# Kernel optimization log

Hardware: AMD Instinct MI355X
Metric: run time of the kernel (lower is better)

Reference implementation:

```python
import jax, jax.numpy as jnp
import numpy as np
import math

B, S, E, H = 2, 2048, 1024, 16
HD = E // H          # head_dim = 64
HX = 64              # helix_dim
P = HX // 2          # helix pairs = 32

def setup_inputs() -> dict:
    key = jax.random.key(0)
    ks = jax.random.split(key, 12)
    sc = 0.02
    return {
        "x":    jax.random.normal(ks[0], (B, S, E), dtype=jnp.float32),
        "Wq":   jax.random.normal(ks[1], (E, E), dtype=jnp.float32) * sc,
        "bq":   jnp.zeros((E,), dtype=jnp.float32),
        "Wk":   jax.random.normal(ks[2], (E, E), dtype=jnp.float32) * sc,
        "bk":   jnp.zeros((E,), dtype=jnp.float32),
        "Wv":   jax.random.normal(ks[3], (E, E), dtype=jnp.float32) * sc,
        "bv":   jnp.zeros((E,), dtype=jnp.float32),
        "Wo":   jax.random.normal(ks[4], (E, E), dtype=jnp.float32) * sc,
        "bo":   jnp.zeros((E,), dtype=jnp.float32),
        "Whel": jax.random.normal(ks[5], (H, HX, HD), dtype=jnp.float32) * sc,
        "bhel": jnp.zeros((H, HX), dtype=jnp.float32),
    }

def _l2norm(x, eps=1e-12):
    # torch F.normalize(p=2, dim=-1): x / max(||x||, eps)
    n = jnp.sqrt(jnp.sum(x * x, axis=-1, keepdims=True))
    return x / jnp.maximum(n, eps)

def _scramble(t):
    # faithful to torch: (B,S,2) -> transpose(1,2) -> reshape(B,S,2),
    # vectorized over (H,P): t is (B,H,P,S,2)
    b, h, p, s, _ = t.shape
    return jnp.swapaxes(t, -1, -2).reshape(b, h, p, s, 2)

def reference(x, Wq, bq, Wk, bk, Wv, bv, Wo, bo, Whel, bhel):
    b, s, e = x.shape
    h, hx, hd = Whel.shape
    p = hx // 2
    q = x @ Wq.T + bq
    k = x @ Wk.T + bk
    v = x @ Wv.T + bv
    qh = q.reshape(b, s, h, hd)
    kh = k.reshape(b, s, h, hd)
    # per-head helical projections: (B,S,H,HX)
    q_hel = jnp.einsum('bshd,hed->bshe', qh, Whel) + bhel
    k_hel = jnp.einsum('bshd,hed->bshe', kh, Whel) + bhel
    # split into 2D coords, normalize each pair: (B,H,P,S,2)
    qn = _l2norm(q_hel.reshape(b, s, h, p, 2)).transpose(0, 2, 3, 1, 4)
    kn = _l2norm(k_hel.reshape(b, s, h, p, 2)).transpose(0, 2, 3, 1, 4)
    qn = _scramble(qn)
    kn = _scramble(kn)
    # helical similarity averaged over pairs: (B,H,S,S)
    helical = jnp.einsum('bhpsc,bhptc->bhst', qn, kn) / p
    # standard scaled dot-product scores
    dot = jnp.einsum('bshd,bthd->bhst', qh, kh) / math.sqrt(hd)
    alpha = 0.5
    attn = jax.nn.softmax(alpha * dot + (1.0 - alpha) * helical, axis=-1)
    vh = v.reshape(b, s, h, hd)
    out = jnp.einsum('bhst,bthd->bshd', attn, vh).reshape(b, s, e)
    return out @ Wo.T + bo
```

## Files before the change

### kernel.cpp

```cpp
#include <hip/hip_runtime.h>
#include <hip/hip_bf16.h>


typedef unsigned short u16;
typedef unsigned int u32;
typedef __attribute__((ext_vector_type(8))) __bf16 bf16x8;
typedef __attribute__((ext_vector_type(4))) float f32x4;
typedef __attribute__((ext_vector_type(16))) float f32x16;

__device__ __forceinline__ u16 f2b(float f) {
  u32 u = __float_as_uint(f);
  u32 r = (u + 0x7fffu + ((u >> 16) & 1u)) >> 16;
  return (u16)r;
}
__device__ __forceinline__ float b2f(u16 h) {
  return __uint_as_float(((u32)h) << 16);
}

__device__ __forceinline__ f32x4 mfma16(bf16x8 a, bf16x8 b, f32x4 c) {
  return __builtin_amdgcn_mfma_f32_16x16x32_bf16(a, b, c, 0, 0, 0);
}
__device__ __forceinline__ f32x16 mfma32(bf16x8 a, bf16x8 b, f32x16 c) {
  return __builtin_amdgcn_mfma_f32_32x32x16_bf16(a, b, c, 0, 0, 0);
}

__device__ __forceinline__ void gld16(void* lds, const void* g) {
  __builtin_amdgcn_global_load_lds(
      (const __attribute__((address_space(1))) unsigned int*)g,
      (__attribute__((address_space(3))) unsigned int*)lds, 16, 0, 0);
}

#define LOG2E 1.4426950408889634f

__global__ __launch_bounds__(256) void cast_kernel(
    const float* __restrict__ x,  const float* __restrict__ wq,
    const float* __restrict__ wk, const float* __restrict__ wv,
    const float* __restrict__ wo, const float* __restrict__ whel,
    u16* __restrict__ xb, u16* __restrict__ wb, u16* __restrict__ wob,
    u16* __restrict__ whb) {
  long long q = (long long)blockIdx.x * 256 + threadIdx.x;
  const float* s; u16* d; long long base;
  if (q < 1048576)      { s = x;    d = xb;            base = 0; }
  else if (q < 1310720) { s = wq;   d = wb;            base = 1048576; }
  else if (q < 1572864) { s = wk;   d = wb + 1048576;  base = 1310720; }
  else if (q < 1835008) { s = wv;   d = wb + 2097152;  base = 1572864; }
  else if (q < 2097152) { s = wo;   d = wob;           base = 1835008; }
  else                  { s = whel; d = whb;           base = 2097152; }
  long long e = (q - base) * 4;
  float4 v = *(const float4*)(s + e);
  ushort4 o;
  o.x = f2b(v.x); o.y = f2b(v.y); o.z = f2b(v.z); o.w = f2b(v.w);
  *(ushort4*)(d + e) = o;
}

__global__ __launch_bounds__(256, 2) void qkv_gemm(
    const u16* __restrict__ xb, const u16* __restrict__ wb,
    const float* __restrict__ bq, const float* __restrict__ bk,
    const float* __restrict__ bv,
    u16* __restrict__ Qcat, u16* __restrict__ Kcat, u16* __restrict__ vt) {
  __shared__ u16 Al[128][32];
  __shared__ u16 Bl[128][32];
  __shared__ u16 T[64][136];
  const int nt = blockIdx.x, mt = blockIdx.y;
  const int which = nt >> 3;
  const int n0 = (nt & 7) << 7;
  const int m0 = mt << 7;
  const int tid = threadIdx.x;
  const int wave = tid >> 6, lane = tid & 63;
  const int g = lane >> 4, c15 = lane & 15;
  const int wm = wave & 1, wn = wave >> 1;
  const u16* Wp = wb + (long long)which * (1024 * 1024) + n0 * 1024;
  const u16* Ap = xb + m0 * 1024;
  const int srow = (wave * 64 + lane) >> 2;
  const int scol = (lane & 3) << 3;

  f32x4 acc[4][4];
#pragma unroll
  for (int i = 0; i < 4; i++)
#pragma unroll
    for (int j = 0; j < 4; j++) acc[i][j] = f32x4{0.f, 0.f, 0.f, 0.f};

  for (int k0 = 0; k0 < 1024; k0 += 32) {
    gld16(&Al[srow][scol],      Ap + srow * 1024 + k0 + scol);
    gld16(&Al[64 + srow][scol], Ap + (64 + srow) * 1024 + k0 + scol);
    gld16(&Bl[srow][scol],      Wp + srow * 1024 + k0 + scol);
    gld16(&Bl[64 + srow][scol], Wp + (64 + srow) * 1024 + k0 + scol);
    __syncthreads();
    bf16x8 a[4], b[4];
#pragma unroll
    for (int i = 0; i < 4; i++)
      a[i] = *(const bf16x8*)&Al[wm * 64 + i * 16 + c15][g * 8];
#pragma unroll
    for (int j = 0; j < 4; j++)
      b[j] = *(const bf16x8*)&Bl[wn * 64 + j * 16 + c15][g * 8];
#pragma unroll
    for (int i = 0; i < 4; i++)
#pragma unroll
      for (int j = 0; j < 4; j++) acc[i][j] = mfma16(a[i], b[j], acc[i][j]);
    __syncthreads();
  }

  if (which == 2) {
#pragma unroll
    for (int half = 0; half < 2; ++half) {
      __syncthreads();
      if (wn == half) {
#pragma unroll
        for (int i = 0; i < 4; i++)
#pragma unroll
          for (int j = 0; j < 4; j++)
#pragma unroll
            for (int r = 0; r < 4; r++) {
              int nloc = j * 16 + c15;
              int mloc = wm * 64 + i * 16 + g * 4 + r;
              float v = acc[i][j][r] + bv[n0 + half * 64 + nloc];
              T[nloc][mloc] = f2b(v);
            }
      }
      __syncthreads();
#pragma unroll
      for (int it = 0; it < 4; ++it) {
        int idx = it * 256 + tid;
        int row = idx >> 4;
        int cm = (idx & 15) * 8;
        int col = n0 + half * 64 + row;
        int hh = col >> 6, dd = col & 63;
        int m = m0 + cm;
        int bb2 = m >> 11, s = m & 2047;
        *(uint4*)&vt[(((bb2 * 16 + hh) * 64) + dd) * 2048 + s] =
            *(const uint4*)&T[row][cm];
      }
    }
    return;
  }

  const float* bias = (which == 0) ? bq : bk;
#pragma unroll
  for (int i = 0; i < 4; i++)
#pragma unroll
    for (int j = 0; j < 4; j++)
#pragma unroll
      for (int r = 0; r < 4; r++) {
        int row = m0 + wm * 64 + i * 16 + g * 4 + r;
        int col = n0 + wn * 64 + j * 16 + c15;
        float v = acc[i][j][r] + bias[col];
        int bb = row >> 11, s = row & 2047;
        int hh = col >> 6, d = col & 63;
        if (which == 0) {
          Qcat[(((bb * 16 + hh) * 2048) + s) * 128 + d] =
              f2b(v * (0.0625f * LOG2E));
        } else {
          Kcat[(((bb * 16 + hh) * 2048) + s) * 128 + d] = f2b(v);
        }
      }
}

__global__ __launch_bounds__(256, 2) void helical_kernel(
    u16* __restrict__ Qcat, u16* __restrict__ Kcat,
    const u16* __restrict__ whb, const float* __restrict__ bhel) {
  __shared__ u16 A[2][2][64][32];
  __shared__ u16 Wl[2][64][32];
  const int sb = blockIdx.x, bh = blockIdx.y;
  const int h = bh & 15;
  const int s0 = sb << 6;
  const int tid = threadIdx.x;
  const int wave = tid >> 6, lane = tid & 63;
  const int g = lane >> 4, c15 = lane & 15;
  u16* Qb = Qcat + (long long)bh * (2048 * 128);
  u16* Kb = Kcat + (long long)bh * (2048 * 128);

#pragma unroll
  for (int it = 0; it < 2; ++it) {
    int cidx = it * 256 + tid;
    int e = cidx >> 3, ds = (cidx & 7) << 3;
    uint4 vv = *(const uint4*)(whb + h * 4096 + e * 64 + ds);
    *(uint4*)&Wl[ds >> 5][e][ds & 31] = vv;
  }
#pragma unroll
  for (int it = 0; it < 4; ++it) {
    int cidx = it * 256 + tid;
    int which = cidx >> 9;
    int r = (cidx >> 3) & 63;
    int ds = (cidx & 7) << 3;
    const u16* src = (which ? Kb : Qb) + (s0 + r) * 128 + ds;
    uint4 vv = *(const uint4*)src;
    if (which == 0) {
      u16 tmp[8];
      *(uint4*)tmp = vv;
#pragma unroll
      for (int q = 0; q < 8; ++q)
        tmp[q] = f2b(b2f(tmp[q]) * (16.0f / LOG2E));
      vv = *(uint4*)tmp;
    }
    *(uint4*)&A[which][ds >> 5][r][ds & 31] = vv;
  }
  __syncthreads();

  const int which = wave >> 1, hf = wave & 1;
  f32x4 acc[2][4];
#pragma unroll
  for (int i = 0; i < 2; i++)
#pragma unroll
    for (int j = 0; j < 4; j++) acc[i][j] = f32x4{0.f, 0.f, 0.f, 0.f};
#pragma unroll
  for (int kq = 0; kq < 2; ++kq) {
    bf16x8 a0 = *(const bf16x8*)&A[which][kq][hf * 32 + c15][g * 8];
    bf16x8 a1 = *(const bf16x8*)&A[which][kq][hf * 32 + 16 + c15][g * 8];
#pragma unroll
    for (int j = 0; j < 4; ++j) {
      bf16x8 bb = *(const bf16x8*)&Wl[kq][j * 16 + c15][g * 8];
      acc[0][j] = mfma16(a0, bb, acc[0][j]);
      acc[1][j] = mfma16(a1, bb, acc[1][j]);
    }
  }
  u16* Dst = which ? Kb : Qb;
  const float oscale = which ? 0.125f : (0.125f * LOG2E);
#pragma unroll
  for (int i = 0; i < 2; ++i)
#pragma unroll
    for (int j = 0; j < 4; ++j)
#pragma unroll
      for (int r = 0; r < 4; ++r) {
        int s_loc = hf * 32 + i * 16 + g * 4 + r;
        int e = j * 16 + c15;
        float v = acc[i][j][r] + bhel[h * 64 + e];
        float pp = __shfl_xor(v, 1);
        float nn = sqrtf(v * v + pp * pp);
        float o = v / fmaxf(nn, 1e-12f) * oscale;
        int s = s0 + s_loc;
        int u = s >> 1, c2 = s & 1;
        int row_out = ((e & 1) ? 1024 : 0) + u;
        int col_out = 64 + (e & ~1) + c2;
        Dst[row_out * 128 + col_out] = f2b(o);
      }
}

__global__ __launch_bounds__(256, 4) void attn_kernel(
    const u16* __restrict__ Qcat, const u16* __restrict__ Kcat,
    const u16* __restrict__ vt, u16* __restrict__ AO) {
  __shared__ u16 Kl[4][64][32];
  __shared__ u16 Vl[2][64][32];
  __shared__ u16 Pl[64][68];
  __shared__ float denl[2][64];
  const int qt = blockIdx.x, bh = blockIdx.y;
  const int bb = bh >> 4, h = bh & 15;
  const int q0 = qt << 6;
  const int tid = threadIdx.x;
  const int w = tid >> 6, lane = tid & 63;
  const int wq = w & 1, wt = w >> 1;
  const int l31 = lane & 31, l5 = lane >> 5;
  const u16* Qb = Qcat + (long long)bh * (2048 * 128);
  const u16* Kb = Kcat + (long long)bh * (2048 * 128);
  const u16* Vb = vt + (long long)bh * (64 * 2048);

  const int srow = lane >> 2;
  const int sc = lane & 3;

  bf16x8 qf[8];
  {
    const u16* qrow = Qb + (q0 + 32 * wq + l31) * 128 + l5 * 8;
#pragma unroll
    for (int ks = 0; ks < 8; ++ks) qf[ks] = *(const bf16x8*)(qrow + ks * 16);
  }

  f32x16 accO;
#pragma unroll
  for (int i = 0; i < 16; ++i) accO[i] = 0.f;
  float den = 0.f;

  for (int t = 0; t < 32; ++t) {
    const int t0 = t << 6;
#pragma unroll
    for (int rg = 0; rg < 4; ++rg) {
      int row = rg * 16 + srow;
      int cc = sc ^ ((row >> 1) & 3);
      gld16(((u16*)Kl) + w * 2048 + rg * 512 + lane * 8,
            Kb + (t0 + row) * 128 + w * 32 + cc * 8);
    }
    {
      int drow = w * 16 + srow;
      int cc = sc ^ ((drow >> 1) & 3);
#pragma unroll
      for (int tq = 0; tq < 2; ++tq)
        gld16(((u16*)Vl) + tq * 2048 + w * 512 + lane * 8,
              Vb + drow * 2048 + t0 + tq * 32 + cc * 8);
    }
    __syncthreads();

    f32x16 accS;
#pragma unroll
    for (int i = 0; i < 16; ++i) accS[i] = 0.f;
    {
      const int row = 32 * wt + l31;
      const int sw = (row >> 1) & 3;
#pragma unroll
      for (int ks = 0; ks < 8; ++ks) {
        int cp = (2 * (ks & 1) + l5) ^ sw;
        bf16x8 ak = *(const bf16x8*)&Kl[ks >> 1][row][cp * 8];
        accS = mfma32(ak, qf[ks], accS);
      }
    }

#pragma unroll
    for (int rr = 0; rr < 4; ++rr) {
      u16 pk[4];
#pragma unroll
      for (int r2 = 0; r2 < 4; ++r2) {
        float p = __builtin_amdgcn_exp2f(accS[rr * 4 + r2]);
        den += p;
        pk[r2] = (u16)(__float_as_uint(p) >> 16);
      }
      *(uint2*)&Pl[32 * wq + l31][32 * wt + 8 * rr + 4 * l5] =
          *(const uint2*)pk;
    }
    __syncthreads();

    {
      const int drow = 32 * wt + l31;
      const int sw = (drow >> 1) & 3;
#pragma unroll
      for (int ks = 0; ks < 4; ++ks) {
        bf16x8 ap = *(const bf16x8*)&Pl[32 * wq + l31][ks * 16 + l5 * 8];
        int ct = 2 * ks + l5;
        bf16x8 bvf = *(const bf16x8*)&Vl[ct >> 2][drow][((ct & 3) ^ sw) * 8];
        accO = mfma32(ap, bvf, accO);
      }
    }
    __syncthreads();
  }

  den += __shfl_xor(den, 32);
  if (lane < 32) denl[wt][32 * wq + lane] = den;
  __syncthreads();

#pragma unroll
  for (int r = 0; r < 16; ++r) {
    int q_loc = 32 * wq + (r & 3) + 8 * (r >> 2) + 4 * l5;
    float dfull = denl[0][q_loc] + denl[1][q_loc];
    float o = accO[r] / dfull;
    int q = q0 + q_loc;
    int d = h * 64 + 32 * wt + l31;
    AO[((bb * 2048 + q) * 1024) + d] = f2b(o);
  }
}

__global__ __launch_bounds__(256, 2) void out_gemm(
    const u16* __restrict__ AO, const u16* __restrict__ wob,
    const float* __restrict__ bo, float* __restrict__ out) {
  __shared__ u16 Al[128][32];
  __shared__ u16 Bl[128][32];
  const int n0 = blockIdx.x << 7;
  const int m0 = blockIdx.y << 7;
  const int tid = threadIdx.x;
  const int wave = tid >> 6, lane = tid & 63;
  const int g = lane >> 4, c15 = lane & 15;
  const int wm = wave & 1, wn = wave >> 1;
  const u16* Wp = wob + n0 * 1024;
  const u16* Ap = AO + m0 * 1024;
  const int srow = (wave * 64 + lane) >> 2;
  const int scol = (lane & 3) << 3;

  f32x4 acc[4][4];
#pragma unroll
  for (int i = 0; i < 4; i++)
#pragma unroll
    for (int j = 0; j < 4; j++) acc[i][j] = f32x4{0.f, 0.f, 0.f, 0.f};

  for (int k0 = 0; k0 < 1024; k0 += 32) {
    gld16(&Al[srow][scol],      Ap + srow * 1024 + k0 + scol);
    gld16(&Al[64 + srow][scol], Ap + (64 + srow) * 1024 + k0 + scol);
    gld16(&Bl[srow][scol],      Wp + srow * 1024 + k0 + scol);
    gld16(&Bl[64 + srow][scol], Wp + (64 + srow) * 1024 + k0 + scol);
    __syncthreads();
    bf16x8 a[4], b[4];
#pragma unroll
    for (int i = 0; i < 4; i++)
      a[i] = *(const bf16x8*)&Al[wm * 64 + i * 16 + c15][g * 8];
#pragma unroll
    for (int j = 0; j < 4; j++)
      b[j] = *(const bf16x8*)&Bl[wn * 64 + j * 16 + c15][g * 8];
#pragma unroll
    for (int i = 0; i < 4; i++)
#pragma unroll
      for (int j = 0; j < 4; j++) acc[i][j] = mfma16(a[i], b[j], acc[i][j]);
    __syncthreads();
  }
#pragma unroll
  for (int i = 0; i < 4; i++)
#pragma unroll
    for (int j = 0; j < 4; j++)
#pragma unroll
      for (int r = 0; r < 4; r++) {
        int row = m0 + wm * 64 + i * 16 + g * 4 + r;
        int col = n0 + wn * 64 + j * 16 + c15;
        out[row * 1024 + col] = acc[i][j][r] + bo[col];
      }
}

extern "C" void kernel_launch(void* const* d_in, const int* in_sizes, int n_in,
                              void* d_out, int out_size, void* d_ws,
                              size_t ws_size, hipStream_t stream) {
  const float* x    = (const float*)d_in[0];
  const float* Wq   = (const float*)d_in[1];
  const float* bq   = (const float*)d_in[2];
  const float* Wk   = (const float*)d_in[3];
  const float* bk   = (const float*)d_in[4];
  const float* Wv   = (const float*)d_in[5];
  const float* bv   = (const float*)d_in[6];
  const float* Wo   = (const float*)d_in[7];
  const float* bo   = (const float*)d_in[8];
  const float* Whel = (const float*)d_in[9];
  const float* bhel = (const float*)d_in[10];
  float* out = (float*)d_out;

  char* ws = (char*)d_ws;
  u16* xb   = (u16*)(ws + 0);
  u16* wb   = (u16*)(ws + 8388608);
  u16* wob  = (u16*)(ws + 14680064);
  u16* whb  = (u16*)(ws + 16777216);
  u16* Qcat = (u16*)(ws + 16908288);
  u16* Kcat = (u16*)(ws + 33685504);
  u16* vt   = (u16*)(ws + 50462720);
  u16* AO   = (u16*)(ws + 58851328);

  dim3 blk(256);
  cast_kernel<<<dim3(8256), blk, 0, stream>>>(x, Wq, Wk, Wv, Wo, Whel, xb, wb,
                                              wob, whb);
  qkv_gemm<<<dim3(24, 32), blk, 0, stream>>>(xb, wb, bq, bk, bv, Qcat, Kcat,
                                             vt);
  helical_kernel<<<dim3(32, 32), blk, 0, stream>>>(Qcat, Kcat, whb, bhel);
  attn_kernel<<<dim3(32, 32), blk, 0, stream>>>(Qcat, Kcat, vt, AO);
  out_gemm<<<dim3(8, 32), blk, 0, stream>>>(AO, wob, bo, out);
}
```

Before: 236.0 us.

## Double-buffer GEMM and attention tiles, keep P in registers via lane shuffles

Both GEMMs now double-buffer their LDS A/B tiles, prefetching the next k-slice after a single barrier per iteration. The attention kernel moves to 512-thread blocks covering 128 queries with double-buffered K/V tiles and a new XOR swizzle. It builds the PV operand from the exponentiated score registers using cross-half-wave shuffles instead of an LDS round trip, and reduces partial outputs across two wave groups through shared memory at the end. This targets global-load latency and barrier and LDS traffic, at the cost of more LDS per block and possibly lower occupancy.

```diff
diff --git a/kernel.cpp b/kernel.cpp
--- a/kernel.cpp
+++ b/kernel.cpp
@@ -7,6 +7,8 @@
 typedef __attribute__((ext_vector_type(8))) __bf16 bf16x8;
 typedef __attribute__((ext_vector_type(4))) float f32x4;
 typedef __attribute__((ext_vector_type(16))) float f32x16;
+
+union BFrag { u32 u[4]; bf16x8 b; };
 
 __device__ __forceinline__ u16 f2b(float f) {
   u32 u = __float_as_uint(f);
@@ -53,13 +55,13 @@
   *(ushort4*)(d + e) = o;
 }
 
-__global__ __launch_bounds__(256, 2) void qkv_gemm(
+__global__ __launch_bounds__(256, 3) void qkv_gemm(
     const u16* __restrict__ xb, const u16* __restrict__ wb,
     const float* __restrict__ bq, const float* __restrict__ bk,
     const float* __restrict__ bv,
     u16* __restrict__ Qcat, u16* __restrict__ Kcat, u16* __restrict__ vt) {
-  __shared__ u16 Al[128][32];
-  __shared__ u16 Bl[128][32];
+  __shared__ u16 Al[2][128][32];
+  __shared__ u16 Bl[2][128][32];
   __shared__ u16 T[64][136];
   const int nt = blockIdx.x, mt = blockIdx.y;
   const int which = nt >> 3;
@@ -80,24 +82,32 @@
 #pragma unroll
     for (int j = 0; j < 4; j++) acc[i][j] = f32x4{0.f, 0.f, 0.f, 0.f};
 
+  gld16(&Al[0][srow][scol],      Ap + srow * 1024 + scol);
+  gld16(&Al[0][64 + srow][scol], Ap + (64 + srow) * 1024 + scol);
+  gld16(&Bl[0][srow][scol],      Wp + srow * 1024 + scol);
+  gld16(&Bl[0][64 + srow][scol], Wp + (64 + srow) * 1024 + scol);
+
   for (int k0 = 0; k0 < 1024; k0 += 32) {
-    gld16(&Al[srow][scol],      Ap + srow * 1024 + k0 + scol);
-    gld16(&Al[64 + srow][scol], Ap + (64 + srow) * 1024 + k0 + scol);
-    gld16(&Bl[srow][scol],      Wp + srow * 1024 + k0 + scol);
-    gld16(&Bl[64 + srow][scol], Wp + (64 + srow) * 1024 + k0 + scol);
+    const int c = (k0 >> 5) & 1;
     __syncthreads();
+    if (k0 + 32 < 1024) {
+      const int kn = k0 + 32;
+      gld16(&Al[c ^ 1][srow][scol],      Ap + srow * 1024 + kn + scol);
+      gld16(&Al[c ^ 1][64 + srow][scol], Ap + (64 + srow) * 1024 + kn + scol);
+      gld16(&Bl[c ^ 1][srow][scol],      Wp + srow * 1024 + kn + scol);
+      gld16(&Bl[c ^ 1][64 + srow][scol], Wp + (64 + srow) * 1024 + kn + scol);
+    }
     bf16x8 a[4], b[4];
 #pragma unroll
     for (int i = 0; i < 4; i++)
-      a[i] = *(const bf16x8*)&Al[wm * 64 + i * 16 + c15][g * 8];
+      a[i] = *(const bf16x8*)&Al[c][wm * 64 + i * 16 + c15][g * 8];
 #pragma unroll
     for (int j = 0; j < 4; j++)
-      b[j] = *(const bf16x8*)&Bl[wn * 64 + j * 16 + c15][g * 8];
+      b[j] = *(const bf16x8*)&Bl[c][wn * 64 + j * 16 + c15][g * 8];
 #pragma unroll
     for (int i = 0; i < 4; i++)
 #pragma unroll
       for (int j = 0; j < 4; j++) acc[i][j] = mfma16(a[i], b[j], acc[i][j]);
-    __syncthreads();
   }
 
   if (which == 2) {
@@ -235,27 +245,23 @@
       }
 }
 
-__global__ __launch_bounds__(256, 4) void attn_kernel(
+__global__ __launch_bounds__(512, 4) void attn_kernel(
     const u16* __restrict__ Qcat, const u16* __restrict__ Kcat,
     const u16* __restrict__ vt, u16* __restrict__ AO) {
-  __shared__ u16 Kl[4][64][32];
-  __shared__ u16 Vl[2][64][32];
-  __shared__ u16 Pl[64][68];
-  __shared__ float denl[2][64];
+  __shared__ u16 Kl[2][64][128];
+  __shared__ u16 Vl[2][64][64];
+  __shared__ float denl[2][128];
   const int qt = blockIdx.x, bh = blockIdx.y;
   const int bb = bh >> 4, h = bh & 15;
-  const int q0 = qt << 6;
+  const int q0 = qt << 7;
   const int tid = threadIdx.x;
   const int w = tid >> 6, lane = tid & 63;
-  const int wq = w & 1, wt = w >> 1;
+  const int wq = w & 3, wt = w >> 2;
   const int l31 = lane & 31, l5 = lane >> 5;
   const u16* Qb = Qcat + (long long)bh * (2048 * 128);
   const u16* Kb = Kcat + (long long)bh * (2048 * 128);
   const u16* Vb = vt + (long long)bh * (64 * 2048);
 
-  const int srow = lane >> 2;
-  const int sc = lane & 3;
-
   bf16x8 qf[8];
   {
     const u16* qrow = Qb + (q0 + 32 * wq + l31) * 128 + l5 * 8;
@@ -263,92 +269,128 @@
     for (int ks = 0; ks < 8; ++ks) qf[ks] = *(const bf16x8*)(qrow + ks * 16);
   }
 
-  f32x16 accO;
-#pragma unroll
-  for (int i = 0; i < 16; ++i) accO[i] = 0.f;
+  const int ll = tid;
+  const int krow0 = ll >> 4;
+  const int kp = ll & 15;
+  const int ksrc0 = (kp & 8) | ((kp & 7) ^ (krow0 & 7));
+  const int krow1 = 32 + krow0;
+  const int ksrc1 = (kp & 8) | ((kp & 7) ^ (krow1 & 7));
+  const int vd = ll >> 3;
+  const int vsrc = (ll & 7) ^ (vd & 7);
+
+  gld16(((u16*)Kl[0]) + ll * 8,        Kb + krow0 * 128 + ksrc0 * 8);
+  gld16(((u16*)Kl[0]) + 4096 + ll * 8, Kb + krow1 * 128 + ksrc1 * 8);
+  gld16(((u16*)Vl[0]) + ll * 8,        Vb + vd * 2048 + vsrc * 8);
+
+  f32x16 accO0, accO1;
+#pragma unroll
+  for (int i = 0; i < 16; ++i) { accO0[i] = 0.f; accO1[i] = 0.f; }
   float den = 0.f;
 
+  const int krow = 32 * wt + l31;
+  const int kr7 = krow & 7;
+
   for (int t = 0; t < 32; ++t) {
-    const int t0 = t << 6;
-#pragma unroll
-    for (int rg = 0; rg < 4; ++rg) {
-      int row = rg * 16 + srow;
-      int cc = sc ^ ((row >> 1) & 3);
-      gld16(((u16*)Kl) + w * 2048 + rg * 512 + lane * 8,
-            Kb + (t0 + row) * 128 + w * 32 + cc * 8);
-    }
+    const int cur = t & 1;
+    __syncthreads();
+    if (t + 1 < 32) {
+      const int t1 = (t + 1) << 6;
+      u16* Kd = (u16*)Kl[cur ^ 1];
+      gld16(Kd + ll * 8,        Kb + (t1 + krow0) * 128 + ksrc0 * 8);
+      gld16(Kd + 4096 + ll * 8, Kb + (t1 + krow1) * 128 + ksrc1 * 8);
+      gld16(((u16*)Vl[cur ^ 1]) + ll * 8, Vb + vd * 2048 + t1 + vsrc * 8);
+    }
+
+    f32x16 accS;
+#pragma unroll
+    for (int i = 0; i < 16; ++i) accS[i] = 0.f;
+#pragma unroll
+    for (int ks = 0; ks < 8; ++ks) {
+      int lc = 2 * ks + l5;
+      int p = (lc & 8) | ((lc & 7) ^ kr7);
+      bf16x8 ak = *(const bf16x8*)&Kl[cur][krow][p * 8];
+      accS = mfma32(ak, qf[ks], accS);
+    }
+
+    u32 D0[2], D1[2], D2[2], D3[2];
+#pragma unroll
+    for (int rr = 0; rr < 4; ++rr) {
+      float p0 = __builtin_amdgcn_exp2f(accS[4 * rr + 0]);
+      float p1 = __builtin_amdgcn_exp2f(accS[4 * rr + 1]);
+      float p2 = __builtin_amdgcn_exp2f(accS[4 * rr + 2]);
+      float p3 = __builtin_amdgcn_exp2f(accS[4 * rr + 3]);
+      den += (p0 + p1) + (p2 + p3);
+      u32 lo = (__float_as_uint(p0) >> 16) | (__float_as_uint(p1) & 0xffff0000u);
+      u32 hi = (__float_as_uint(p2) >> 16) | (__float_as_uint(p3) & 0xffff0000u);
+      if (rr == 0) { D0[0] = lo; D0[1] = hi; }
+      else if (rr == 1) { D1[0] = lo; D1[1] = hi; }
+      else if (rr == 2) { D2[0] = lo; D2[1] = hi; }
+      else { D3[0] = lo; D3[1] = hi; }
+    }
+    BFrag A0, A1;
     {
-      int drow = w * 16 + srow;
-      int cc = sc ^ ((drow >> 1) & 3);
-#pragma unroll
-      for (int tq = 0; tq < 2; ++tq)
-        gld16(((u16*)Vl) + tq * 2048 + w * 512 + lane * 8,
-              Vb + drow * 2048 + t0 + tq * 32 + cc * 8);
-    }
-    __syncthreads();
-
-    f32x16 accS;
-#pragma unroll
-    for (int i = 0; i < 16; ++i) accS[i] = 0.f;
-    {
-      const int row = 32 * wt + l31;
-      const int sw = (row >> 1) & 3;
-#pragma unroll
-      for (int ks = 0; ks < 8; ++ks) {
-        int cp = (2 * (ks & 1) + l5) ^ sw;
-        bf16x8 ak = *(const bf16x8*)&Kl[ks >> 1][row][cp * 8];
-        accS = mfma32(ak, qf[ks], accS);
-      }
-    }
-
-#pragma unroll
-    for (int rr = 0; rr < 4; ++rr) {
-      u16 pk[4];
-#pragma unroll
-      for (int r2 = 0; r2 < 4; ++r2) {
-        float p = __builtin_amdgcn_exp2f(accS[rr * 4 + r2]);
-        den += p;
-        pk[r2] = (u16)(__float_as_uint(p) >> 16);
-      }
-      *(uint2*)&Pl[32 * wq + l31][32 * wt + 8 * rr + 4 * l5] =
-          *(const uint2*)pk;
-    }
-    __syncthreads();
-
-    {
-      const int drow = 32 * wt + l31;
-      const int sw = (drow >> 1) & 3;
-#pragma unroll
-      for (int ks = 0; ks < 4; ++ks) {
-        bf16x8 ap = *(const bf16x8*)&Pl[32 * wq + l31][ks * 16 + l5 * 8];
-        int ct = 2 * ks + l5;
-        bf16x8 bvf = *(const bf16x8*)&Vl[ct >> 2][drow][((ct & 3) ^ sw) * 8];
-        accO = mfma32(ap, bvf, accO);
-      }
-    }
-    __syncthreads();
+      u32 e00 = __shfl_xor((int)D0[0], 32), e01 = __shfl_xor((int)D0[1], 32);
+      u32 e10 = __shfl_xor((int)D1[0], 32), e11 = __shfl_xor((int)D1[1], 32);
+      u32 e20 = __shfl_xor((int)D2[0], 32), e21 = __shfl_xor((int)D2[1], 32);
+      u32 e30 = __shfl_xor((int)D3[0], 32), e31 = __shfl_xor((int)D3[1], 32);
+      A0.u[0] = l5 ? e10 : D0[0];
+      A0.u[1] = l5 ? e11 : D0[1];
+      A0.u[2] = l5 ? D1[0] : e00;
+      A0.u[3] = l5 ? D1[1] : e01;
+      A1.u[0] = l5 ? e30 : D2[0];
+      A1.u[1] = l5 ? e31 : D2[1];
+      A1.u[2] = l5 ? D3[0] : e20;
+      A1.u[3] = l5 ? D3[1] : e21;
+    }
+
+#pragma unroll
+    for (int dq = 0; dq < 2; ++dq) {
+      int d = 32 * dq + l31;
+      int d7 = d & 7;
+#pragma unroll
+      for (int ks = 0; ks < 2; ++ks) {
+        int lc = 4 * wt + 2 * ks + l5;
+        bf16x8 bvf = *(const bf16x8*)&Vl[cur][d][((lc ^ d7) & 7) * 8];
+        if (dq == 0) accO0 = mfma32(ks ? A1.b : A0.b, bvf, accO0);
+        else         accO1 = mfma32(ks ? A1.b : A0.b, bvf, accO1);
+      }
+    }
   }
 
   den += __shfl_xor(den, 32);
   if (lane < 32) denl[wt][32 * wq + lane] = den;
   __syncthreads();
 
-#pragma unroll
-  for (int r = 0; r < 16; ++r) {
-    int q_loc = 32 * wq + (r & 3) + 8 * (r >> 2) + 4 * l5;
-    float dfull = denl[0][q_loc] + denl[1][q_loc];
-    float o = accO[r] / dfull;
-    int q = q0 + q_loc;
-    int d = h * 64 + 32 * wt + l31;
-    AO[((bb * 2048 + q) * 1024) + d] = f2b(o);
+  float* S = (float*)Kl;
+  if (wt == 1) {
+#pragma unroll
+    for (int r = 0; r < 16; ++r) {
+      int qr = (r & 3) + 8 * (r >> 2) + 4 * l5;
+      S[(wq * 32 + qr) * 64 + l31] = accO0[r];
+      S[(wq * 32 + qr) * 64 + 32 + l31] = accO1[r];
+    }
+  }
+  __syncthreads();
+  if (wt == 0) {
+#pragma unroll
+    for (int r = 0; r < 16; ++r) {
+      int qr = (r & 3) + 8 * (r >> 2) + 4 * l5;
+      int ql = 32 * wq + qr;
+      float inv = 1.0f / (denl[0][ql] + denl[1][ql]);
+      float o0 = (accO0[r] + S[(wq * 32 + qr) * 64 + l31]) * inv;
+      float o1 = (accO1[r] + S[(wq * 32 + qr) * 64 + 32 + l31]) * inv;
+      long long base = ((long long)(bb * 2048 + q0 + ql) * 1024) + h * 64;
+      AO[base + l31] = f2b(o0);
+      AO[base + 32 + l31] = f2b(o1);
+    }
   }
 }
 
 __global__ __launch_bounds__(256, 2) void out_gemm(
     const u16* __restrict__ AO, const u16* __restrict__ wob,
     const float* __restrict__ bo, float* __restrict__ out) {
-  __shared__ u16 Al[128][32];
-  __shared__ u16 Bl[128][32];
+  __shared__ u16 Al[2][128][32];
+  __shared__ u16 Bl[2][128][32];
   const int n0 = blockIdx.x << 7;
   const int m0 = blockIdx.y << 7;
   const int tid = threadIdx.x;
@@ -366,24 +408,32 @@
 #pragma unroll
     for (int j = 0; j < 4; j++) acc[i][j] = f32x4{0.f, 0.f, 0.f, 0.f};
 
+  gld16(&Al[0][srow][scol],      Ap + srow * 1024 + scol);
+  gld16(&Al[0][64 + srow][scol], Ap + (64 + srow) * 1024 + scol);
+  gld16(&Bl[0][srow][scol],      Wp + srow * 1024 + scol);
+  gld16(&Bl[0][64 + srow][scol], Wp + (64 + srow) * 1024 + scol);
+
   for (int k0 = 0; k0 < 1024; k0 += 32) {
-    gld16(&Al[srow][scol],      Ap + srow * 1024 + k0 + scol);
-    gld16(&Al[64 + srow][scol], Ap + (64 + srow) * 1024 + k0 + scol);
-    gld16(&Bl[srow][scol],      Wp + srow * 1024 + k0 + scol);
-    gld16(&Bl[64 + srow][scol], Wp + (64 + srow) * 1024 + k0 + scol);
+    const int c = (k0 >> 5) & 1;
     __syncthreads();
+    if (k0 + 32 < 1024) {
+      const int kn = k0 + 32;
+      gld16(&Al[c ^ 1][srow][scol],      Ap + srow * 1024 + kn + scol);
+      gld16(&Al[c ^ 1][64 + srow][scol], Ap + (64 + srow) * 1024 + kn + scol);
+      gld16(&Bl[c ^ 1][srow][scol],      Wp + srow * 1024 + kn + scol);
+      gld16(&Bl[c ^ 1][64 + srow][scol], Wp + (64 + srow) * 1024 + kn + scol);
+    }
     bf16x8 a[4], b[4];
 #pragma unroll
     for (int i = 0; i < 4; i++)
-      a[i] = *(const bf16x8*)&Al[wm * 64 + i * 16 + c15][g * 8];
+      a[i] = *(const bf16x8*)&Al[c][wm * 64 + i * 16 + c15][g * 8];
 #pragma unroll
     for (int j = 0; j < 4; j++)
-      b[j] = *(const bf16x8*)&Bl[wn * 64 + j * 16 + c15][g * 8];
+      b[j] = *(const bf16x8*)&Bl[c][wn * 64 + j * 16 + c15][g * 8];
 #pragma unroll
     for (int i = 0; i < 4; i++)
 #pragma unroll
       for (int j = 0; j < 4; j++) acc[i][j] = mfma16(a[i], b[j], acc[i][j]);
-    __syncthreads();
   }
 #pragma unroll
   for (int i = 0; i < 4; i++)
@@ -423,12 +473,12 @@
   u16* vt   = (u16*)(ws + 50462720);
   u16* AO   = (u16*)(ws + 58851328);
 
-  dim3 blk(256);
-  cast_kernel<<<dim3(8256), blk, 0, stream>>>(x, Wq, Wk, Wv, Wo, Whel, xb, wb,
-                                              wob, whb);
-  qkv_gemm<<<dim3(24, 32), blk, 0, stream>>>(xb, wb, bq, bk, bv, Qcat, Kcat,
-                                             vt);
-  helical_kernel<<<dim3(32, 32), blk, 0, stream>>>(Qcat, Kcat, whb, bhel);
-  attn_kernel<<<dim3(32, 32), blk, 0, stream>>>(Qcat, Kcat, vt, AO);
-  out_gemm<<<dim3(8, 32), blk, 0, stream>>>(AO, wob, bo, out);
-}
+  cast_kernel<<<dim3(8256), dim3(256), 0, stream>>>(x, Wq, Wk, Wv, Wo, Whel,
+                                                    xb, wb, wob, whb);
+  qkv_gemm<<<dim3(24, 32), dim3(256), 0, stream>>>(xb, wb, bq, bk, bv, Qcat,
+                                                   Kcat, vt);
+  helical_kernel<<<dim3(32, 32), dim3(256), 0, stream>>>(Qcat, Kcat, whb,
+                                                         bhel);
+  attn_kernel<<<dim3(16, 32), dim3(512), 0, stream>>>(Qcat, Kcat, vt, AO);
+  out_gemm<<<dim3(8, 32), dim3(256), 0, stream>>>(AO, wob, bo, out);
+}
```

New measurement: 226.4 us. 4.1% less time.
